# Performance work log

Hardware: AMD Instinct MI355X
Metric: run time of the kernel (lower is better)

The kernel has to match this reference:

```python
import jax, jax.numpy as jnp
import numpy as np

MS_KS = 9
C = 256
BN_EPS = 1e-5


def setup_inputs() -> dict:
    key = jax.random.key(0)
    k1, k2, k3 = jax.random.split(key, 3)
    p2_r = jax.random.normal(k1, (2, C, 64, 128), dtype=jnp.float32)
    conv_w = jax.random.normal(k2, (C, C, 1, MS_KS), dtype=jnp.float32) * 0.02
    conv1_w = jax.random.normal(k3, (1, C, 1, 1), dtype=jnp.float32) * 0.05
    bn_gamma = jnp.ones((1,), jnp.float32)
    bn_beta = jnp.zeros((1,), jnp.float32)
    return dict(p2_r=p2_r, conv_w=conv_w, conv1_w=conv1_w,
                bn_gamma=bn_gamma, bn_beta=bn_beta)


def _scnn_pass(x, M):
    # x: [b,c,h,w]. Each step applies conv(1,ms_ks) to a width-1 column with
    # zero padding ms_ks//2 -> only the center tap contributes, i.e. a 256x256
    # channel matmul per column, followed by relu and residual add.
    cols = jnp.moveaxis(x, 3, 0)  # [w,b,c,h]
    def step(carry, col):
        new = col + jax.nn.relu(jnp.einsum('oc,bch->boh', M, carry))
        return new, new
    _, outs = jax.lax.scan(step, cols[0], cols[1:])
    outs = jnp.concatenate([cols[:1], outs], axis=0)[::-1]  # mirrors out[::-1]
    return jnp.moveaxis(outs, 0, 3)


def _upsample_bilinear_ac(x, factor=4):
    # F.interpolate(mode='bilinear', align_corners=True)
    b, c, h, w = x.shape
    Ho, Wo = factor * h, factor * w
    ys = jnp.arange(Ho, dtype=x.dtype) * ((h - 1) / (Ho - 1))
    xs = jnp.arange(Wo, dtype=x.dtype) * ((w - 1) / (Wo - 1))
    y0 = jnp.floor(ys).astype(jnp.int32)
    y1 = jnp.minimum(y0 + 1, h - 1)
    wy = (ys - y0.astype(x.dtype))[None, None, :, None]
    rows = x[:, :, y0, :] * (1 - wy) + x[:, :, y1, :] * wy  # [b,c,Ho,w]
    x0 = jnp.floor(xs).astype(jnp.int32)
    x1 = jnp.minimum(x0 + 1, w - 1)
    wx = (xs - x0.astype(x.dtype))[None, None, None, :]
    return rows[:, :, :, x0] * (1 - wx) + rows[:, :, :, x1] * wx


def reference(p2_r, conv_w, conv1_w, bn_gamma, bn_beta):
    M = conv_w[:, :, 0, MS_KS // 2]  # center tap, [c_out, c_in]
    x = _scnn_pass(p2_r, M)                     # reverse=False
    x = _scnn_pass(x[:, :, :, ::-1], M)         # reverse=True (slices[::-1])
    x = _upsample_bilinear_ac(x, 4)             # [b,256,4h,4w]
    x = jnp.einsum('oc,bchw->bohw', conv1_w[:, :, 0, 0], x)  # 1x1 conv -> 1 ch
    # BatchNorm2d(1), training-mode batch statistics (biased variance)
    mean = jnp.mean(x, axis=(0, 2, 3), keepdims=True)
    var = jnp.mean((x - mean) ** 2, axis=(0, 2, 3), keepdims=True)
    x = (x - mean) * jax.lax.rsqrt(var + BN_EPS)
    x = x * bn_gamma[None, :, None, None] + bn_beta[None, :, None, None]
    return jax.nn.sigmoid(x)
```

## Files before the change

kernel.cpp:

```cpp
#include <hip/hip_runtime.h>


typedef _Float16 f16x8 __attribute__((ext_vector_type(8)));
typedef _Float16 f16x4 __attribute__((ext_vector_type(4)));
typedef float    f32x4 __attribute__((ext_vector_type(4)));

extern "C" __global__ void k_extract(const float* __restrict__ convw,
                                     _Float16* __restrict__ Md) {
  int q = blockIdx.x * 256 + threadIdx.x;
  float4 v = ((const float4*)convw)[q];
  float vv[4] = {v.x, v.y, v.z, v.w};
  int f = q * 4;
#pragma unroll
  for (int e = 0; e < 4; ++e) {
    int flat = f + e;
    if (flat % 9 == 4) Md[flat / 9] = (_Float16)vv[e];
  }
}

struct SM {
  _Float16 cy[2][256];
  _Float16 pad_[32];
  _Float16 cz[2][256];
  float    sp[128 * 32];
  float    cbuf[2][256][20];
};

extern "C" __global__ void __launch_bounds__(512, 2)
k_scan(const float* __restrict__ p2, const _Float16* __restrict__ Md,
       const float* __restrict__ conv1, float* __restrict__ sout,
       float* __restrict__ stats, unsigned int* __restrict__ cnt) {
  __shared__ SM sm;
  const int tid  = threadIdx.x;
  const int l    = tid & 63;
  const int r    = tid >> 6;
  const int col  = l & 15;
  const int quad = l >> 4;
  const int b    = blockIdx.x >> 6;
  const int h    = blockIdx.x & 63;

  if (blockIdx.x == 0 && tid == 0) { stats[0] = 0.f; stats[1] = 0.f; *cnt = 0u; }

  const bool isY = (col == 0);
  const bool isZ = (col == 1);

  const int m0 = r * 32 + quad * 4;
  const int m1 = m0 + 16;

  const int ch0 = tid >> 2;
  const int q4  = (tid & 3) * 4;

  const float* pbase = p2 + (size_t)b * 2097152 + (size_t)h * 128;

  {
    float4 g0 = *(const float4*)(pbase + (size_t)ch0 * 8192 + q4);
    float4 g1 = *(const float4*)(pbase + (size_t)(ch0 + 128) * 8192 + q4);
    *(float4*)(&sm.cbuf[0][ch0][q4])       = g0;
    *(float4*)(&sm.cbuf[0][ch0 + 128][q4]) = g1;
  }

  f16x8 A0[8], A1[8];
#pragma unroll
  for (int ch = 0; ch < 8; ++ch) {
    A0[ch] = *(const f16x8*)(Md + (size_t)(r * 32 + col) * 256 + ch * 32 + quad * 8);
    A1[ch] = *(const f16x8*)(Md + (size_t)(r * 32 + col + 16) * 256 + ch * 32 + quad * 8);
  }

  float vva[4], vvb[4];
  if (isZ) {
#pragma unroll
    for (int i = 0; i < 4; ++i) { vva[i] = conv1[m0 + i]; vvb[i] = conv1[m1 + i]; }
  }
  __syncthreads();

  if (isY || isZ) {
    float c0a[4], c0b[4];
#pragma unroll
    for (int i = 0; i < 4; ++i) {
      c0a[i] = sm.cbuf[0][m0 + i][0];
      c0b[i] = sm.cbuf[0][m1 + i][0];
    }
    if (isY) {
      f16x4 pa, pb;
#pragma unroll
      for (int i = 0; i < 4; ++i) { pa[i] = (_Float16)c0a[i]; pb[i] = (_Float16)c0b[i]; }
      *(f16x4*)(sm.cy[0] + m0) = pa; *(f16x4*)(sm.cy[0] + m1) = pb;
      *(f16x4*)(sm.cz[0] + m0) = pa; *(f16x4*)(sm.cz[0] + m1) = pb;
    }
    if (isZ) {
      float p = 0.f;
#pragma unroll
      for (int i = 0; i < 4; ++i) p += vva[i] * c0a[i] + vvb[i] * c0b[i];
      sm.sp[0 * 32 + r * 4 + quad] = p;
    }
  }
  __syncthreads();

  const _Float16* selA = ((l & 1) ? sm.cz[0] : sm.cy[0]) + quad * 8;
  const _Float16* selB = ((l & 1) ? sm.cz[1] : sm.cy[1]) + quad * 8;

#define STEP(W, SELP, WY, WZ, DOSTAGE)                                         \
  do {                                                                         \
          \
    float4 g0, g1; int t1 = 0; bool stg = false;                               \
    if (DOSTAGE) {                                                             \
      stg = (((W) & 15) == 1) && ((W) < 113);                                  \
      if (stg) {                                                               \
        t1 = ((W) >> 4) + 1;                                                   \
        g0 = *(const float4*)(pbase + (size_t)ch0 * 8192 + t1 * 16 + q4);      \
        g1 = *(const float4*)(pbase + (size_t)(ch0 + 128) * 8192 + t1 * 16 + q4);\
      }                                                                        \
    }                                                                          \
    f16x8 B[8];                                                                \
    _Pragma("unroll")                                                          \
    for (int ch = 0; ch < 8; ++ch)                                             \
      B[ch] = *(const f16x8*)((SELP) + ch * 32);                               \
    f32x4 a00 = {0.f,0.f,0.f,0.f}, a01 = {0.f,0.f,0.f,0.f};                    \
    f32x4 a10 = {0.f,0.f,0.f,0.f}, a11 = {0.f,0.f,0.f,0.f};                    \
    _Pragma("unroll")                                                          \
    for (int ch = 0; ch < 4; ++ch) {                                           \
      a00 = __builtin_amdgcn_mfma_f32_16x16x32_f16(A0[ch],   B[ch],   a00,0,0,0);\
      a10 = __builtin_amdgcn_mfma_f32_16x16x32_f16(A1[ch],   B[ch],   a10,0,0,0);\
      a01 = __builtin_amdgcn_mfma_f32_16x16x32_f16(A0[ch+4], B[ch+4], a01,0,0,0);\
      a11 = __builtin_amdgcn_mfma_f32_16x16x32_f16(A1[ch+4], B[ch+4], a11,0,0,0);\
    }                                                                          \
    f32x4 acc0 = a00 + a01, acc1 = a10 + a11;                                  \
    if (DOSTAGE && stg) {                                                      \
      float* dst = &sm.cbuf[t1 & 1][0][0];                                     \
      *(float4*)(dst + ch0 * 20 + q4)         = g0;                            \
      *(float4*)(dst + (ch0 + 128) * 20 + q4) = g1;                            \
    }                                                                          \
    const float* cptr = &sm.cbuf[((W) >> 4) & 1][0][(W) & 15];                 \
    f16x4 yh0 = {}, yh1 = {};                                                  \
    if (isY) {                                                                 \
      _Pragma("unroll")                                                        \
      for (int i = 0; i < 4; ++i) {                                            \
        yh0[i] = (_Float16)(cptr[(m0 + i) * 20] + fmaxf(acc0[i], 0.f));        \
        yh1[i] = (_Float16)(cptr[(m1 + i) * 20] + fmaxf(acc1[i], 0.f));        \
      }                                                                        \
      *(f16x4*)((WY) + m0) = yh0;                                              \
      *(f16x4*)((WY) + m1) = yh1;                                              \
    }                                                                          \
    int2 u0 = __builtin_bit_cast(int2, yh0), u1 = __builtin_bit_cast(int2, yh1);\
    u0.x = __shfl(u0.x, l & 62, 64); u0.y = __shfl(u0.y, l & 62, 64);          \
    u1.x = __shfl(u1.x, l & 62, 64); u1.y = __shfl(u1.y, l & 62, 64);          \
    f16x4 ys0 = __builtin_bit_cast(f16x4, u0), ys1 = __builtin_bit_cast(f16x4, u1);\
    if (isZ) {                                                                 \
      f16x4 zh0, zh1;                                                          \
      float p = 0.f;                                                           \
      _Pragma("unroll")                                                        \
      for (int i = 0; i < 4; ++i) {                                            \
        float z0 = (float)ys0[i] + fmaxf(acc0[i], 0.f);                        \
        float z1 = (float)ys1[i] + fmaxf(acc1[i], 0.f);                        \
        zh0[i] = (_Float16)z0; zh1[i] = (_Float16)z1;                          \
        p += vva[i] * z0 + vvb[i] * z1;                                        \
      }                                                                        \
      *(f16x4*)((WZ) + m0) = zh0;                                              \
      *(f16x4*)((WZ) + m1) = zh1;                                              \
      sm.sp[(W) * 32 + r * 4 + quad] = p;                                      \
    }                                                                          \
    __syncthreads();                                                           \
  } while (0)

#pragma unroll 1
  for (int w = 1; w < 127; w += 2) {
    STEP(w,     selA, sm.cy[1], sm.cz[1], 1);
    STEP(w + 1, selB, sm.cy[0], sm.cz[0], 0);
  }
  STEP(127, selA, sm.cy[1], sm.cz[1], 0);
#undef STEP

  if (tid < 128) {
    const float4* q = (const float4*)(sm.sp + tid * 32);
    float s = 0.f;
#pragma unroll
    for (int j = 0; j < 8; ++j) { float4 t4 = q[j]; s += t4.x + t4.y + t4.z + t4.w; }
    sout[(blockIdx.x << 7) + (127 - tid)] = s;
  }
}

static __device__ __forceinline__ float bilin(const float* __restrict__ s,
                                              int idx) {
  int bb  = idx >> 17;
  int rem = idx & 131071;
  int ho  = rem >> 9;
  int wo  = rem & 511;
  const float SY = 63.0f / 255.0f, SX = 127.0f / 511.0f;
  float fy = (float)ho * SY;
  int y0 = (int)fy; int y1 = min(y0 + 1, 63); float wy = fy - (float)y0;
  float fx = (float)wo * SX;
  int x0 = (int)fx; int x1 = min(x0 + 1, 127); float wx = fx - (float)x0;
  const float* sb = s + bb * 8192;
  float cA = sb[y0 * 128 + x0] * (1.f - wy) + sb[y1 * 128 + x0] * wy;
  float cB = sb[y0 * 128 + x1] * (1.f - wy) + sb[y1 * 128 + x1] * wy;
  return cA * (1.f - wx) + cB * wx;
}

extern "C" __global__ void __launch_bounds__(256, 1)
k_statsnorm(const float* __restrict__ s, float* __restrict__ stats,
            unsigned int* __restrict__ cnt, const float* __restrict__ gamma,
            const float* __restrict__ beta, float* __restrict__ out) {
  int tid  = threadIdx.x;
  int base = blockIdx.x * 1024 + tid;
  float u[4];
  float sum = 0.f, ssq = 0.f;
#pragma unroll
  for (int i = 0; i < 4; ++i) {
    u[i] = bilin(s, base + i * 256);
    sum += u[i]; ssq += u[i] * u[i];
  }
#pragma unroll
  for (int off = 32; off > 0; off >>= 1) {
    sum += __shfl_xor(sum, off, 64);
    ssq += __shfl_xor(ssq, off, 64);
  }
  __shared__ float ls[4], lq[4];
  int wv = tid >> 6;
  if ((tid & 63) == 0) { ls[wv] = sum; lq[wv] = ssq; }
  __syncthreads();
  if (tid == 0) {
    float bsum = ls[0] + ls[1] + ls[2] + ls[3];
    float bssq = lq[0] + lq[1] + lq[2] + lq[3];
    __hip_atomic_fetch_add(&stats[0], bsum, __ATOMIC_RELAXED, __HIP_MEMORY_SCOPE_AGENT);
    __hip_atomic_fetch_add(&stats[1], bssq, __ATOMIC_RELAXED, __HIP_MEMORY_SCOPE_AGENT);
    __hip_atomic_fetch_add(cnt, 1u, __ATOMIC_RELEASE, __HIP_MEMORY_SCOPE_AGENT);
    while (__hip_atomic_load(cnt, __ATOMIC_ACQUIRE, __HIP_MEMORY_SCOPE_AGENT) < 256u)
      __builtin_amdgcn_s_sleep(8);
  }
  __syncthreads();
  float s0 = __hip_atomic_load(&stats[0], __ATOMIC_RELAXED, __HIP_MEMORY_SCOPE_AGENT);
  float s1 = __hip_atomic_load(&stats[1], __ATOMIC_RELAXED, __HIP_MEMORY_SCOPE_AGENT);
  const float invN = 1.f / 262144.f;
  float mean  = s0 * invN;
  float var   = s1 * invN - mean * mean;
  float scale = rsqrtf(var + 1e-5f) * gamma[0];
  float bias  = beta[0] - mean * scale;
#pragma unroll
  for (int i = 0; i < 4; ++i) {
    float x = u[i] * scale + bias;
    out[base + i * 256] = 1.f / (1.f + __expf(-x));
  }
}

extern "C" void kernel_launch(void* const* d_in, const int* in_sizes, int n_in,
                              void* d_out, int out_size, void* d_ws, size_t ws_size,
                              hipStream_t stream) {
  const float* p2    = (const float*)d_in[0];
  const float* convw = (const float*)d_in[1];
  const float* conv1 = (const float*)d_in[2];
  const float* gamma = (const float*)d_in[3];
  const float* beta  = (const float*)d_in[4];
  float* out = (float*)d_out;

  char* ws = (char*)d_ws;
  float*        s     = (float*)ws;
  float*        stats = (float*)(ws + 65536);
  unsigned int* cnt   = (unsigned int*)(ws + 65544);
  _Float16*     Md    = (_Float16*)(ws + 65792);

  hipLaunchKernelGGL(k_extract,   dim3(576), dim3(256), 0, stream, convw, Md);
  hipLaunchKernelGGL(k_scan,      dim3(128), dim3(512), 0, stream,
                     p2, Md, conv1, s, stats, cnt);
  hipLaunchKernelGGL(k_statsnorm, dim3(256), dim3(256), 0, stream,
                     s, stats, cnt, gamma, beta, out);
}
```

Before: 198.3 us.

## Halve scan block to 4 waves with 64 rows each, transpose column buffer

The per-row scan kernel now uses 256 threads (4 waves) instead of 512. Each wave owns 64 output channels via four 16-row MFMA tiles held in registers, and every lane now applies the residual and ReLU. The column staging buffer is transposed to [w][channel] so residual values are read as contiguous vectors. The pair exchange uses a DPP swap instead of a generic shuffle. Fewer waves per barrier should cut sync cost on this latency-bound sequential loop, at the price of higher register pressure (128 A-operand VGPRs per lane) and less MFMA parallelism per step.

```diff
diff --git a/kernel.cpp b/kernel.cpp
--- a/kernel.cpp
+++ b/kernel.cpp
@@ -4,6 +4,14 @@
 typedef _Float16 f16x8 __attribute__((ext_vector_type(8)));
 typedef _Float16 f16x4 __attribute__((ext_vector_type(4)));
 typedef float    f32x4 __attribute__((ext_vector_type(4)));
+
+static __device__ __forceinline__ int xchg_pair(int x) {
+#if __has_builtin(__builtin_amdgcn_update_dpp)
+  return __builtin_amdgcn_update_dpp(x, x, 0xB1, 0xF, 0xF, true);
+#else
+  return __shfl_xor(x, 1, 64);
+#endif
+}
 
 extern "C" __global__ void k_extract(const float* __restrict__ convw,
                                      _Float16* __restrict__ Md) {
@@ -20,13 +28,14 @@
 
 struct SM {
   _Float16 cy[2][256];
-  _Float16 pad_[32];
+  _Float16 pad0[32];
   _Float16 cz[2][256];
-  float    sp[128 * 32];
-  float    cbuf[2][256][20];
+  _Float16 pad1[32];
+  float    cbuf[2][16][256];
+  float    sp[128][20];
 };
 
-extern "C" __global__ void __launch_bounds__(512, 2)
+extern "C" __global__ void __launch_bounds__(256, 1)
 k_scan(const float* __restrict__ p2, const _Float16* __restrict__ Md,
        const float* __restrict__ conv1, float* __restrict__ sout,
        float* __restrict__ stats, unsigned int* __restrict__ cnt) {
@@ -43,55 +52,61 @@
 
   const bool isY = (col == 0);
   const bool isZ = (col == 1);
-
-  const int m0 = r * 32 + quad * 4;
-  const int m1 = m0 + 16;
-
-  const int ch0 = tid >> 2;
-  const int q4  = (tid & 3) * 4;
+  const int  mq  = r * 64 + quad * 4;
 
   const float* pbase = p2 + (size_t)b * 2097152 + (size_t)h * 128;
 
   {
-    float4 g0 = *(const float4*)(pbase + (size_t)ch0 * 8192 + q4);
-    float4 g1 = *(const float4*)(pbase + (size_t)(ch0 + 128) * 8192 + q4);
-    *(float4*)(&sm.cbuf[0][ch0][q4])       = g0;
-    *(float4*)(&sm.cbuf[0][ch0 + 128][q4]) = g1;
-  }
-
-  f16x8 A0[8], A1[8];
-#pragma unroll
-  for (int ch = 0; ch < 8; ++ch) {
-    A0[ch] = *(const f16x8*)(Md + (size_t)(r * 32 + col) * 256 + ch * 32 + quad * 8);
-    A1[ch] = *(const f16x8*)(Md + (size_t)(r * 32 + col + 16) * 256 + ch * 32 + quad * 8);
-  }
-
-  float vva[4], vvb[4];
-  if (isZ) {
-#pragma unroll
-    for (int i = 0; i < 4; ++i) { vva[i] = conv1[m0 + i]; vvb[i] = conv1[m1 + i]; }
-  }
-  __syncthreads();
-
-  if (isY || isZ) {
-    float c0a[4], c0b[4];
-#pragma unroll
-    for (int i = 0; i < 4; ++i) {
-      c0a[i] = sm.cbuf[0][m0 + i][0];
-      c0b[i] = sm.cbuf[0][m1 + i][0];
+    const f32x4* g = (const f32x4*)(pbase + (size_t)tid * 8192);
+    f32x4 g0 = g[0], g1 = g[1], g2 = g[2], g3 = g[3];
+#pragma unroll
+    for (int j = 0; j < 4; ++j) {
+      sm.cbuf[0][j][tid]      = g0[j];
+      sm.cbuf[0][4 + j][tid]  = g1[j];
+      sm.cbuf[0][8 + j][tid]  = g2[j];
+      sm.cbuf[0][12 + j][tid] = g3[j];
     }
+  }
+
+  f16x8 A[4][8];
+#pragma unroll
+  for (int t = 0; t < 4; ++t)
+#pragma unroll
+    for (int ch = 0; ch < 8; ++ch)
+      A[t][ch] = *(const f16x8*)(Md + (size_t)(r * 64 + t * 16 + col) * 256 +
+                                 ch * 32 + quad * 8);
+
+  float vvf[16];
+#pragma unroll
+  for (int t = 0; t < 4; ++t) {
+    f32x4 vt = *(const f32x4*)(conv1 + mq + t * 16);
+#pragma unroll
+    for (int i = 0; i < 4; ++i) vvf[t * 4 + i] = vt[i];
+  }
+  __syncthreads();
+
+  {
+    f32x4 c0[4];
+#pragma unroll
+    for (int t = 0; t < 4; ++t)
+      c0[t] = *(const f32x4*)(&sm.cbuf[0][0][mq + t * 16]);
     if (isY) {
-      f16x4 pa, pb;
-#pragma unroll
-      for (int i = 0; i < 4; ++i) { pa[i] = (_Float16)c0a[i]; pb[i] = (_Float16)c0b[i]; }
-      *(f16x4*)(sm.cy[0] + m0) = pa; *(f16x4*)(sm.cy[0] + m1) = pb;
-      *(f16x4*)(sm.cz[0] + m0) = pa; *(f16x4*)(sm.cz[0] + m1) = pb;
+#pragma unroll
+      for (int t = 0; t < 4; ++t) {
+        f16x4 p;
+#pragma unroll
+        for (int i = 0; i < 4; ++i) p[i] = (_Float16)c0[t][i];
+        *(f16x4*)(sm.cy[0] + mq + t * 16) = p;
+        *(f16x4*)(sm.cz[0] + mq + t * 16) = p;
+      }
     }
     if (isZ) {
       float p = 0.f;
 #pragma unroll
-      for (int i = 0; i < 4; ++i) p += vva[i] * c0a[i] + vvb[i] * c0b[i];
-      sm.sp[0 * 32 + r * 4 + quad] = p;
+      for (int t = 0; t < 4; ++t)
+#pragma unroll
+        for (int i = 0; i < 4; ++i) p += vvf[t * 4 + i] * c0[t][i];
+      sm.sp[0][r * 4 + quad] = p;
     }
   }
   __syncthreads();
@@ -101,63 +116,76 @@
 
 #define STEP(W, SELP, WY, WZ, DOSTAGE)                                         \
   do {                                                                         \
-          \
-    float4 g0, g1; int t1 = 0; bool stg = false;                               \
-    if (DOSTAGE) {                                                             \
-      stg = (((W) & 15) == 1) && ((W) < 113);                                  \
-      if (stg) {                                                               \
-        t1 = ((W) >> 4) + 1;                                                   \
-        g0 = *(const float4*)(pbase + (size_t)ch0 * 8192 + t1 * 16 + q4);      \
-        g1 = *(const float4*)(pbase + (size_t)(ch0 + 128) * 8192 + t1 * 16 + q4);\
-      }                                                                        \
+    f32x4 g0, g1, g2, g3;                                                      \
+    bool stg = (DOSTAGE) && (((W) & 15) == 1) && ((W) < 113);                  \
+    int t1 = ((W) >> 4) + 1;                                                   \
+    if (stg) {                                                                 \
+      const f32x4* g = (const f32x4*)(pbase + (size_t)tid * 8192 + t1 * 16);   \
+      g0 = g[0]; g1 = g[1]; g2 = g[2]; g3 = g[3];                              \
     }                                                                          \
     f16x8 B[8];                                                                \
     _Pragma("unroll")                                                          \
     for (int ch = 0; ch < 8; ++ch)                                             \
       B[ch] = *(const f16x8*)((SELP) + ch * 32);                               \
-    f32x4 a00 = {0.f,0.f,0.f,0.f}, a01 = {0.f,0.f,0.f,0.f};                    \
-    f32x4 a10 = {0.f,0.f,0.f,0.f}, a11 = {0.f,0.f,0.f,0.f};                    \
-    _Pragma("unroll")                                                          \
-    for (int ch = 0; ch < 4; ++ch) {                                           \
-      a00 = __builtin_amdgcn_mfma_f32_16x16x32_f16(A0[ch],   B[ch],   a00,0,0,0);\
-      a10 = __builtin_amdgcn_mfma_f32_16x16x32_f16(A1[ch],   B[ch],   a10,0,0,0);\
-      a01 = __builtin_amdgcn_mfma_f32_16x16x32_f16(A0[ch+4], B[ch+4], a01,0,0,0);\
-      a11 = __builtin_amdgcn_mfma_f32_16x16x32_f16(A1[ch+4], B[ch+4], a11,0,0,0);\
-    }                                                                          \
-    f32x4 acc0 = a00 + a01, acc1 = a10 + a11;                                  \
-    if (DOSTAGE && stg) {                                                      \
-      float* dst = &sm.cbuf[t1 & 1][0][0];                                     \
-      *(float4*)(dst + ch0 * 20 + q4)         = g0;                            \
-      *(float4*)(dst + (ch0 + 128) * 20 + q4) = g1;                            \
-    }                                                                          \
-    const float* cptr = &sm.cbuf[((W) >> 4) & 1][0][(W) & 15];                 \
-    f16x4 yh0 = {}, yh1 = {};                                                  \
+    const float* cb = &sm.cbuf[((W) >> 4) & 1][(W) & 15][0];                   \
+    f32x4 cr[4];                                                               \
+    _Pragma("unroll")                                                          \
+    for (int t = 0; t < 4; ++t)                                                \
+      cr[t] = *(const f32x4*)(cb + mq + t * 16);     \
+    f32x4 acc[4];                                                              \
+    _Pragma("unroll")                                                          \
+    for (int t = 0; t < 4; ++t) {                                              \
+      f32x4 p0 = {0.f, 0.f, 0.f, 0.f}, p1 = {0.f, 0.f, 0.f, 0.f};             \
+      p0 = __builtin_amdgcn_mfma_f32_16x16x32_f16(A[t][0], B[0], p0, 0, 0, 0); \
+      p1 = __builtin_amdgcn_mfma_f32_16x16x32_f16(A[t][4], B[4], p1, 0, 0, 0); \
+      p0 = __builtin_amdgcn_mfma_f32_16x16x32_f16(A[t][1], B[1], p0, 0, 0, 0); \
+      p1 = __builtin_amdgcn_mfma_f32_16x16x32_f16(A[t][5], B[5], p1, 0, 0, 0); \
+      p0 = __builtin_amdgcn_mfma_f32_16x16x32_f16(A[t][2], B[2], p0, 0, 0, 0); \
+      p1 = __builtin_amdgcn_mfma_f32_16x16x32_f16(A[t][6], B[6], p1, 0, 0, 0); \
+      p0 = __builtin_amdgcn_mfma_f32_16x16x32_f16(A[t][3], B[3], p0, 0, 0, 0); \
+      p1 = __builtin_amdgcn_mfma_f32_16x16x32_f16(A[t][7], B[7], p1, 0, 0, 0); \
+      acc[t] = p0 + p1;                                                        \
+    }                                                                          \
+                       \
+    f16x4 yh[4], ys[4];                                                        \
+    _Pragma("unroll")                                                          \
+    for (int t = 0; t < 4; ++t) {                                              \
+      _Pragma("unroll")                                                        \
+      for (int i = 0; i < 4; ++i)                                              \
+        yh[t][i] = (_Float16)(cr[t][i] + fmaxf(acc[t][i], 0.f));               \
+      int2 u = __builtin_bit_cast(int2, yh[t]);                                \
+      u.x = xchg_pair(u.x); u.y = xchg_pair(u.y);                              \
+      ys[t] = __builtin_bit_cast(f16x4, u);      \
+    }                                                                          \
     if (isY) {                                                                 \
       _Pragma("unroll")                                                        \
-      for (int i = 0; i < 4; ++i) {                                            \
-        yh0[i] = (_Float16)(cptr[(m0 + i) * 20] + fmaxf(acc0[i], 0.f));        \
-        yh1[i] = (_Float16)(cptr[(m1 + i) * 20] + fmaxf(acc1[i], 0.f));        \
+      for (int t = 0; t < 4; ++t)                                              \
+        *(f16x4*)((WY) + mq + t * 16) = yh[t];                                 \
+    }                                                                          \
+    if (isZ) {                                                                 \
+      float p = 0.f;                                                           \
+      _Pragma("unroll")                                                        \
+      for (int t = 0; t < 4; ++t) {                                            \
+        f16x4 zh;                                                              \
+        _Pragma("unroll")                                                      \
+        for (int i = 0; i < 4; ++i) {                                          \
+          float z = (float)ys[t][i] + fmaxf(acc[t][i], 0.f);                   \
+          zh[i] = (_Float16)z;                                                 \
+          p += vvf[t * 4 + i] * z;                                             \
+        }                                                                      \
+        *(f16x4*)((WZ) + mq + t * 16) = zh;                                    \
       }                                                                        \
-      *(f16x4*)((WY) + m0) = yh0;                                              \
-      *(f16x4*)((WY) + m1) = yh1;                                              \
-    }                                                                          \
-    int2 u0 = __builtin_bit_cast(int2, yh0), u1 = __builtin_bit_cast(int2, yh1);\
-    u0.x = __shfl(u0.x, l & 62, 64); u0.y = __shfl(u0.y, l & 62, 64);          \
-    u1.x = __shfl(u1.x, l & 62, 64); u1.y = __shfl(u1.y, l & 62, 64);          \
-    f16x4 ys0 = __builtin_bit_cast(f16x4, u0), ys1 = __builtin_bit_cast(f16x4, u1);\
-    if (isZ) {                                                                 \
-      f16x4 zh0, zh1;                                                          \
-      float p = 0.f;                                                           \
-      _Pragma("unroll")                                                        \
-      for (int i = 0; i < 4; ++i) {                                            \
-        float z0 = (float)ys0[i] + fmaxf(acc0[i], 0.f);                        \
-        float z1 = (float)ys1[i] + fmaxf(acc1[i], 0.f);                        \
-        zh0[i] = (_Float16)z0; zh1[i] = (_Float16)z1;                          \
-        p += vva[i] * z0 + vvb[i] * z1;                                        \
+      sm.sp[(W)][r * 4 + quad] = p;                                            \
+    }                                                                          \
+    if (stg) {                                                                 \
+      int bs = t1 & 1;                                                         \
+      _Pragma("unroll")                                                        \
+      for (int j = 0; j < 4; ++j) {                                            \
+        sm.cbuf[bs][j][tid]      = g0[j];                                      \
+        sm.cbuf[bs][4 + j][tid]  = g1[j];                                      \
+        sm.cbuf[bs][8 + j][tid]  = g2[j];                                      \
+        sm.cbuf[bs][12 + j][tid] = g3[j];                                      \
       }                                                                        \
-      *(f16x4*)((WZ) + m0) = zh0;                                              \
-      *(f16x4*)((WZ) + m1) = zh1;                                              \
-      sm.sp[(W) * 32 + r * 4 + quad] = p;                                      \
     }                                                                          \
     __syncthreads();                                                           \
   } while (0)
@@ -171,10 +199,10 @@
 #undef STEP
 
   if (tid < 128) {
-    const float4* q = (const float4*)(sm.sp + tid * 32);
-    float s = 0.f;
-#pragma unroll
-    for (int j = 0; j < 8; ++j) { float4 t4 = q[j]; s += t4.x + t4.y + t4.z + t4.w; }
+    const f32x4* q = (const f32x4*)(sm.sp[tid]);
+    f32x4 q0 = q[0], q1 = q[1], q2 = q[2], q3 = q[3];
+    float s = q0[0] + q0[1] + q0[2] + q0[3] + q1[0] + q1[1] + q1[2] + q1[3] +
+              q2[0] + q2[1] + q2[2] + q2[3] + q3[0] + q3[1] + q3[2] + q3[3];
     sout[(blockIdx.x << 7) + (127 - tid)] = s;
   }
 }
@@ -259,7 +287,7 @@
   _Float16*     Md    = (_Float16*)(ws + 65792);
 
   hipLaunchKernelGGL(k_extract,   dim3(576), dim3(256), 0, stream, convw, Md);
-  hipLaunchKernelGGL(k_scan,      dim3(128), dim3(512), 0, stream,
+  hipLaunchKernelGGL(k_scan,      dim3(128), dim3(256), 0, stream,
                      p2, Md, conv1, s, stats, cnt);
   hipLaunchKernelGGL(k_statsnorm, dim3(256), dim3(256), 0, stream,
                      s, stats, cnt, gamma, beta, out);
```

New measurement: 196.6 us. Within noise of the previous version (-0.9%).
